# Optimization experiments

Hardware: AMD Instinct MI355X
Metric: run time of the kernel (lower is better)

The kernel has to match this reference:

```python
import jax, jax.numpy as jnp
import numpy as np

B, Lq, C, NH, NP, DFF = 8, 10000, 256, 8, 4, 1024
H_IMG, W_IMG = 100, 100
HD = C // NH


def _layer_norm(x, g, b, eps=1e-5):
    m = jnp.mean(x, -1, keepdims=True)
    v = jnp.mean((x - m) ** 2, -1, keepdims=True)
    return (x - m) / jnp.sqrt(v + eps) * g + b


def _bilinear_sample(value, loc, Hs, Ws):
    # value: [B, Lin, NH, HD]; loc: [B, Lq, NH, NP, 2] normalized to [0,1]
    vt = jnp.transpose(value, (0, 2, 1, 3))  # [B, NH, Lin, HD]
    # move to [B, NH, Lq, NP] layout once; grid_sample(align_corners=False) pixel coords
    x = jnp.transpose(loc[..., 0], (0, 2, 1, 3)) * Ws - 0.5
    y = jnp.transpose(loc[..., 1], (0, 2, 1, 3)) * Hs - 0.5
    x0 = jnp.floor(x); y0 = jnp.floor(y)
    lx = x - x0; ly = y - y0

    def corner(xi, yi, w):
        valid = (xi >= 0) & (xi < Ws) & (yi >= 0) & (yi < Hs)
        xc = jnp.clip(xi, 0, Ws - 1).astype(jnp.int32)
        yc = jnp.clip(yi, 0, Hs - 1).astype(jnp.int32)
        idx = (yc * Ws + xc).reshape(B, NH, Lq * NP, 1)
        v = jnp.take_along_axis(vt, idx, axis=2).reshape(B, NH, Lq, NP, HD)
        return v * (w * valid)[..., None]

    acc = corner(x0, y0, (1 - lx) * (1 - ly))
    acc = acc + corner(x0 + 1, y0, lx * (1 - ly))
    acc = acc + corner(x0, y0 + 1, (1 - lx) * ly)
    acc = acc + corner(x0 + 1, y0 + 1, lx * ly)
    return acc  # [B, NH, Lq, NP, HD]


def setup_inputs() -> dict:
    key = jax.random.key(0)
    ks = jax.random.split(key, 12)
    s = 0.02
    return {
        "query": jax.random.normal(ks[0], (B, Lq, C), jnp.float32),
        "src": jax.random.normal(ks[1], (B, H_IMG * W_IMG, C), jnp.float32),
        "reference_points": jax.random.uniform(ks[2], (B, Lq, 1, 2), jnp.float32),
        "spatial_shapes": jnp.array([[H_IMG, W_IMG]], dtype=jnp.int64),
        "level_start_index": jnp.array([0], dtype=jnp.int64),
        "W_off": jax.random.normal(ks[3], (C, NH * NP * 2), jnp.float32) * s,
        "b_off": jnp.zeros((NH * NP * 2,), jnp.float32),
        "W_aw": jax.random.normal(ks[4], (C, NH * NP), jnp.float32) * s,
        "b_aw": jnp.zeros((NH * NP,), jnp.float32),
        "W_val": jax.random.normal(ks[5], (C, C), jnp.float32) * s,
        "b_val": jnp.zeros((C,), jnp.float32),
        "W_out": jax.random.normal(ks[6], (C, C), jnp.float32) * s,
        "b_out": jnp.zeros((C,), jnp.float32),
        "g1": jnp.ones((C,), jnp.float32),
        "be1": jnp.zeros((C,), jnp.float32),
        "W1": jax.random.normal(ks[7], (C, DFF), jnp.float32) * s,
        "b1": jnp.zeros((DFF,), jnp.float32),
        "W2": jax.random.normal(ks[8], (DFF, C), jnp.float32) * s,
        "b2": jnp.zeros((C,), jnp.float32),
        "g2": jnp.ones((C,), jnp.float32),
        "be2": jnp.zeros((C,), jnp.float32),
    }


def reference(query, src, reference_points, spatial_shapes, level_start_index,
              W_off, b_off, W_aw, b_aw, W_val, b_val, W_out, b_out,
              g1, be1, W1, b1, W2, b2, g2, be2):
    Hs = spatial_shapes[0, 0]
    Ws = spatial_shapes[0, 1]
    # MSDeformAttn (n_levels = 1)
    value = (src @ W_val + b_val).reshape(B, -1, NH, HD)
    off = (query @ W_off + b_off).reshape(B, Lq, NH, NP, 2)
    aw = jax.nn.softmax((query @ W_aw + b_aw).reshape(B, Lq, NH, NP), axis=-1)
    normalizer = jnp.stack([Ws, Hs]).astype(query.dtype)  # (W, H)
    loc = reference_points[:, :, None] + off / normalizer  # [B,Lq,NH,NP,2]
    sampled = _bilinear_sample(value, loc, Hs, Ws)  # [B,NH,Lq,NP,HD]
    attn = jnp.einsum('bhqpd,bqhp->bqhd', sampled, aw).reshape(B, Lq, C)
    attn = attn @ W_out + b_out
    # residual + LN + FFN + LN
    q = _layer_norm(query + attn, g1, be1)
    ffn = jax.nn.relu(q @ W1 + b1) @ W2 + b2
    return _layer_norm(q + ffn, g2, be2)
```

## Files before the change

kernel.cpp:

```cpp
#include <hip/hip_runtime.h>
#include <hip/hip_bf16.h>

typedef __hip_bfloat16 bf16;
typedef unsigned short u16;
typedef short short8 __attribute__((ext_vector_type(8)));
typedef float f32x4 __attribute__((ext_vector_type(4)));

static constexpr int B_   = 8;
static constexpr int Lq_  = 10000;
static constexpr int C_   = 256;
static constexpr int NH_  = 8;
static constexpr int NP_  = 4;
static constexpr int DFF_ = 1024;
static constexpr int HIMG = 100;
static constexpr int WIMG = 100;
static constexpr int LIN  = 10000;

__device__ __forceinline__ u16 f2bf(float x) {
    union { bf16 b; u16 u; } cv; cv.b = __float2bfloat16(x); return cv.u;
}
__device__ __forceinline__ float bf2f(u16 u) {
    return __uint_as_float((unsigned)u << 16);
}
__device__ __forceinline__ void stf(float* p, float v) { *p = v; }
__device__ __forceinline__ void stf(u16* p, float v)   { *p = f2bf(v); }

__device__ __forceinline__ void gl_lds16(const void* g, void* l) {
    __builtin_amdgcn_global_load_lds(
        (const __attribute__((address_space(1))) void*)g,
        (__attribute__((address_space(3))) void*)l, 16, 0, 0);
}

template <bool RELU, bool AF32, typename TC>
__global__ __launch_bounds__(256) void gemm_mfma(
    const void* __restrict__ Av, const u16* __restrict__ Bt,
    const float* __restrict__ bias, TC* __restrict__ C,
    int M, int K, int Nreal, int ldc)
{
    __shared__ __align__(16) u16 As[2][128 * 32];
    __shared__ __align__(16) u16 Bs[2][128 * 32];

    const int tid  = threadIdx.x;
    const int lane = tid & 63;
    const int w    = tid >> 6;
    const int wr   = (w >> 1) * 64;
    const int wc   = (w & 1) * 64;
    const int m0   = blockIdx.y * 128;
    const int n0   = blockIdx.x * 128;

    const int srow = lane >> 2;
    const int scol = (lane & 3) << 3;
    const u16* bG = Bt + (size_t)(n0 + w * 32 + srow) * K + scol;
    const size_t rstep16 = (size_t)16 * K;

    const u16*   aG  = nullptr;
    const float* aGf = nullptr;
    int ar = 0, ac = 0;
    if constexpr (AF32) {
        ar  = lane >> 3;
        ac  = (lane & 7) << 2;
        aGf = (const float*)Av + (size_t)(m0 + w * 32 + ar) * K + ac;
    } else {
        aG = (const u16*)Av + (size_t)(m0 + w * 32 + srow) * K + scol;
    }

    const int aRoff = (wr + (lane & 15)) * 32 + (lane >> 4) * 8;
    const int bRoff = (wc + (lane & 15)) * 32 + (lane >> 4) * 8;

    f32x4 acc[4][4];
#pragma unroll
    for (int i = 0; i < 4; ++i)
#pragma unroll
        for (int j = 0; j < 4; ++j) acc[i][j] = f32x4{0.f, 0.f, 0.f, 0.f};

    float4 a4[4];

    const int nt = K >> 5;

    if constexpr (AF32) {
#pragma unroll
        for (int rep = 0; rep < 4; ++rep)
            a4[rep] = *(const float4*)(aGf + (size_t)(rep * 8) * K);
#pragma unroll
        for (int rep = 0; rep < 4; ++rep) {
            ushort4 v{f2bf(a4[rep].x), f2bf(a4[rep].y), f2bf(a4[rep].z), f2bf(a4[rep].w)};
            *(ushort4*)&As[0][(w * 32 + rep * 8 + ar) * 32 + ac] = v;
        }
    } else {
        gl_lds16(aG, &As[0][(w * 32) * 32]);
        gl_lds16(aG + rstep16, &As[0][(w * 32 + 16) * 32]);
    }
    gl_lds16(bG, &Bs[0][(w * 32) * 32]);
    gl_lds16(bG + rstep16, &Bs[0][(w * 32 + 16) * 32]);
    asm volatile("s_waitcnt vmcnt(0) lgkmcnt(0)" ::: "memory");
    __builtin_amdgcn_s_barrier();

    for (int t = 0; t < nt; ++t) {
        const int cur = t & 1;
        const int nxt = cur ^ 1;
        const int k0n = (t + 1) << 5;
        const bool has_next = (t + 1 < nt);

        if (has_next) {
            if constexpr (AF32) {
#pragma unroll
                for (int rep = 0; rep < 4; ++rep)
                    a4[rep] = *(const float4*)(aGf + k0n + (size_t)(rep * 8) * K);
            } else {
                gl_lds16(aG + k0n, &As[nxt][(w * 32) * 32]);
                gl_lds16(aG + k0n + rstep16, &As[nxt][(w * 32 + 16) * 32]);
            }
            gl_lds16(bG + k0n, &Bs[nxt][(w * 32) * 32]);
            gl_lds16(bG + k0n + rstep16, &Bs[nxt][(w * 32 + 16) * 32]);
        }

        short8 af[4], bfr[4];
#pragma unroll
        for (int m = 0; m < 4; ++m) af[m]  = *(const short8*)&As[cur][aRoff + m * 16 * 32];
#pragma unroll
        for (int n = 0; n < 4; ++n) bfr[n] = *(const short8*)&Bs[cur][bRoff + n * 16 * 32];
#pragma unroll
        for (int m = 0; m < 4; ++m)
#pragma unroll
            for (int n = 0; n < 4; ++n)
                acc[m][n] = __builtin_amdgcn_mfma_f32_16x16x32_bf16(
                    af[m], bfr[n], acc[m][n], 0, 0, 0);

        if constexpr (AF32) {
            if (has_next) {
#pragma unroll
                for (int rep = 0; rep < 4; ++rep) {
                    ushort4 v{f2bf(a4[rep].x), f2bf(a4[rep].y), f2bf(a4[rep].z), f2bf(a4[rep].w)};
                    *(ushort4*)&As[nxt][(w * 32 + rep * 8 + ar) * 32 + ac] = v;
                }
            }
        }

        asm volatile("s_waitcnt vmcnt(0) lgkmcnt(0)" ::: "memory");
        __builtin_amdgcn_s_barrier();
    }

#pragma unroll
    for (int n = 0; n < 4; ++n) {
        const int gc = n0 + wc + n * 16 + (lane & 15);
        if (gc >= Nreal) continue;
        const float bv = bias[gc];
        const int gr0 = m0 + wr + (lane >> 4) * 4;
#pragma unroll
        for (int m = 0; m < 4; ++m) {
#pragma unroll
            for (int r = 0; r < 4; ++r) {
                float v = acc[m][n][r] + bv;
                if (RELU) v = fmaxf(v, 0.f);
                stf(&C[(size_t)(gr0 + m * 16 + r) * ldc + gc], v);
            }
        }
    }
}

__global__ __launch_bounds__(256) void prep_all(
    const float* __restrict__ Wv, const float* __restrict__ Wo,
    const float* __restrict__ W1, const float* __restrict__ W2,
    const float* __restrict__ Woff, const float* __restrict__ Waw,
    const float* __restrict__ boff, const float* __restrict__ baw,
    u16* __restrict__ Wv_t, u16* __restrict__ Wo_t,
    u16* __restrict__ W1_t, u16* __restrict__ W2_t,
    u16* __restrict__ Woa_t, float* __restrict__ boa)
{
    const int idx = blockIdx.x * 256 + threadIdx.x;
    if (idx < 65536) {
        const int n = idx >> 8, k = idx & 255;
        Wv_t[idx] = f2bf(Wv[(size_t)k * 256 + n]);
    } else if (idx < 131072) {
        const int i = idx - 65536, n = i >> 8, k = i & 255;
        Wo_t[i] = f2bf(Wo[(size_t)k * 256 + n]);
    } else if (idx < 393216) {
        const int i = idx - 131072, n = i >> 8, k = i & 255;
        W1_t[i] = f2bf(W1[(size_t)k * 1024 + n]);
    } else if (idx < 655360) {
        const int i = idx - 393216, n = i >> 10, k = i & 1023;
        W2_t[i] = f2bf(W2[(size_t)k * 256 + n]);
    } else if (idx < 688128) {
        const int i = idx - 655360, n = i >> 8, k = i & 255;
        float v = 0.f;
        if (n < 64)      v = Woff[(size_t)k * 64 + n];
        else if (n < 96) v = Waw[(size_t)k * 32 + (n - 64)];
        Woa_t[i] = f2bf(v);
    } else if (idx < 688256) {
        const int i = idx - 688128;
        boa[i] = (i < 64) ? boff[i] : (i < 96 ? baw[i - 64] : 0.f);
    }
}

__global__ __launch_bounds__(256) void sample_attn(
    const u16* __restrict__ val, const float* __restrict__ oaw,
    const float* __restrict__ refp, u16* __restrict__ attn)
{
    const int t   = threadIdx.x;
    const int gid = blockIdx.x * 64 + (t >> 2);
    const int c0  = (t & 3) << 3;
    const int h   = gid & (NH_ - 1);
    const int bq  = gid >> 3;

    const float* row = oaw + (size_t)bq * 96;
    const float rx = refp[(size_t)bq * 2 + 0] * (float)WIMG;
    const float ry = refp[(size_t)bq * 2 + 1] * (float)HIMG;

    const float4 aw4 = *(const float4*)(row + 64 + h * 4);
    const float mx = fmaxf(fmaxf(aw4.x, aw4.y), fmaxf(aw4.z, aw4.w));
    const float e0 = __expf(aw4.x - mx), e1 = __expf(aw4.y - mx);
    const float e2 = __expf(aw4.z - mx), e3 = __expf(aw4.w - mx);
    const float inv = 1.f / (e0 + e1 + e2 + e3);
    const float w4[4] = {e0 * inv, e1 * inv, e2 * inv, e3 * inv};

    const int b = bq / Lq_;
    const u16* vb = val + (size_t)b * LIN * C_ + h * 32 + c0;

    float acc[8] = {};
#pragma unroll
    for (int p = 0; p < NP_; ++p) {
        const float2 off = *(const float2*)(row + (h * 4 + p) * 2);
        const float x = rx + off.x - 0.5f;
        const float y = ry + off.y - 0.5f;
        const float xf = floorf(x), yf = floorf(y);
        const float lx = x - xf, ly = y - yf;
        const int x0 = (int)xf, y0 = (int)yf;
        const float wp = w4[p];
        const float w00 = wp * (1.f - lx) * (1.f - ly);
        const float w10 = wp * lx * (1.f - ly);
        const float w01 = wp * (1.f - lx) * ly;
        const float w11 = wp * lx * ly;

#pragma unroll
        for (int c = 0; c < 4; ++c) {
            const int xi = x0 + (c & 1);
            const int yi = y0 + (c >> 1);
            const float wc = (c == 0) ? w00 : (c == 1) ? w10 : (c == 2) ? w01 : w11;
            const bool v = ((unsigned)xi < (unsigned)WIMG) & ((unsigned)yi < (unsigned)HIMG);
            const int idx = v ? (yi * WIMG + xi) : 0;
            const float w = v ? wc : 0.f;
            const short8 d = *(const short8*)(vb + (size_t)idx * C_);
#pragma unroll
            for (int j = 0; j < 8; ++j)
                acc[j] = fmaf(w, bf2f(((const u16*)&d)[j]), acc[j]);
        }
    }

    union { short8 s; u16 u[8]; } o;
#pragma unroll
    for (int j = 0; j < 8; ++j) o.u[j] = f2bf(acc[j]);
    *(short8*)(attn + (size_t)bq * C_ + h * 32 + c0) = o.s;
}

template <bool XF32, bool OUTF32>
__global__ __launch_bounds__(256) void ln_add(
    const void* __restrict__ xp, const u16* __restrict__ y,
    const float* __restrict__ g, const float* __restrict__ be,
    void* __restrict__ outp, int rows)
{
    const int row  = blockIdx.x * 4 + (threadIdx.x >> 6);
    const int lane = threadIdx.x & 63;
    if (row >= rows) return;

    float v[4];
    if constexpr (XF32) {
        const float4 xv = *(const float4*)((const float*)xp + (size_t)row * C_ + (lane << 2));
        v[0] = xv.x; v[1] = xv.y; v[2] = xv.z; v[3] = xv.w;
    } else {
        const ushort4 xv = *(const ushort4*)((const u16*)xp + (size_t)row * C_ + (lane << 2));
        v[0] = bf2f(xv.x); v[1] = bf2f(xv.y); v[2] = bf2f(xv.z); v[3] = bf2f(xv.w);
    }
    const ushort4 yv = *(const ushort4*)(y + (size_t)row * C_ + (lane << 2));
    v[0] += bf2f(yv.x); v[1] += bf2f(yv.y); v[2] += bf2f(yv.z); v[3] += bf2f(yv.w);

    float s  = v[0] + v[1] + v[2] + v[3];
    float s2 = v[0] * v[0] + v[1] * v[1] + v[2] * v[2] + v[3] * v[3];
#pragma unroll
    for (int o = 32; o >= 1; o >>= 1) {
        s  += __shfl_xor(s, o);
        s2 += __shfl_xor(s2, o);
    }
    const float mean = s * (1.f / 256.f);
    const float var  = fmaxf(s2 * (1.f / 256.f) - mean * mean, 0.f);
    const float rstd = rsqrtf(var + 1e-5f);

    const float4 gv = *(const float4*)(g  + (lane << 2));
    const float4 bv = *(const float4*)(be + (lane << 2));
    float o4[4];
    o4[0] = (v[0] - mean) * rstd * gv.x + bv.x;
    o4[1] = (v[1] - mean) * rstd * gv.y + bv.y;
    o4[2] = (v[2] - mean) * rstd * gv.z + bv.z;
    o4[3] = (v[3] - mean) * rstd * gv.w + bv.w;

    if constexpr (OUTF32) {
        float4 ov{o4[0], o4[1], o4[2], o4[3]};
        *(float4*)((float*)outp + (size_t)row * C_ + (lane << 2)) = ov;
    } else {
        ushort4 ov{f2bf(o4[0]), f2bf(o4[1]), f2bf(o4[2]), f2bf(o4[3])};
        *(ushort4*)((u16*)outp + (size_t)row * C_ + (lane << 2)) = ov;
    }
}

extern "C" void kernel_launch(void* const* d_in, const int* in_sizes, int n_in,
                              void* d_out, int out_size, void* d_ws, size_t ws_size,
                              hipStream_t stream)
{
    const float* query = (const float*)d_in[0];
    const float* src   = (const float*)d_in[1];
    const float* refp  = (const float*)d_in[2];
    const float* W_off = (const float*)d_in[5];
    const float* b_off = (const float*)d_in[6];
    const float* W_aw  = (const float*)d_in[7];
    const float* b_aw  = (const float*)d_in[8];
    const float* W_val = (const float*)d_in[9];
    const float* b_val = (const float*)d_in[10];
    const float* W_out = (const float*)d_in[11];
    const float* b_out = (const float*)d_in[12];
    const float* g1    = (const float*)d_in[13];
    const float* be1   = (const float*)d_in[14];
    const float* W1    = (const float*)d_in[15];
    const float* b1    = (const float*)d_in[16];
    const float* W2    = (const float*)d_in[17];
    const float* b2    = (const float*)d_in[18];
    const float* g2    = (const float*)d_in[19];
    const float* be2   = (const float*)d_in[20];
    float* out = (float*)d_out;

    char* ws = (char*)d_ws;
    const int R = B_ * Lq_;

    u16*  val   = (u16*)(ws + 0);
    u16*  ffno  = (u16*)(ws + 0);
    float* oaw  = (float*)(ws + 40960000);
    u16*  h     = (u16*)(ws + 40960000);
    u16*  attn  = (u16*)(ws + 71680000);
    u16*  attno = (u16*)(ws + 112640000);
    u16*  q1b   = (u16*)(ws + 204800000);
    u16*  Wv_t  = (u16*)(ws + 245760000);
    u16*  Wo_t  = (u16*)(ws + 245760000 + 131072);
    u16*  W1_t  = (u16*)(ws + 245760000 + 262144);
    u16*  W2_t  = (u16*)(ws + 245760000 + 786432);
    u16*  Woa_t = (u16*)(ws + 245760000 + 1310720);
    float* boa  = (float*)(ws + 245760000 + 1376256);

    const dim3 blk(256);

    prep_all<<<2689, blk, 0, stream>>>(W_val, W_out, W1, W2, W_off, W_aw,
                                       b_off, b_aw, Wv_t, Wo_t, W1_t, W2_t,
                                       Woa_t, boa);

    gemm_mfma<false, true, u16><<<dim3(2, 625), blk, 0, stream>>>(
        src, Wv_t, b_val, val, R, 256, 256, 256);
    gemm_mfma<false, true, float><<<dim3(1, 625), blk, 0, stream>>>(
        query, Woa_t, boa, oaw, R, 256, 96, 96);
    sample_attn<<<dim3(R * NH_ / 64), blk, 0, stream>>>(val, oaw, refp, attn);
    gemm_mfma<false, false, u16><<<dim3(2, 625), blk, 0, stream>>>(
        attn, Wo_t, b_out, attno, R, 256, 256, 256);
    ln_add<true, false><<<dim3(R / 4), blk, 0, stream>>>(
        query, attno, g1, be1, q1b, R);
    gemm_mfma<true, false, u16><<<dim3(8, 625), blk, 0, stream>>>(
        q1b, W1_t, b1, h, R, 256, 1024, 1024);
    gemm_mfma<false, false, u16><<<dim3(2, 625), blk, 0, stream>>>(
        h, W2_t, b2, ffno, R, 1024, 256, 256);
    ln_add<false, true><<<dim3(R / 4), blk, 0, stream>>>(
        q1b, ffno, g2, be2, out, R);
}
```

Measured before the change: 368.7 us.

## Fuse LayerNorm into GEMM epilogues and fuse FFN into one kernel

Replaces the generic GEMM with a 128x256 full-row tile kernel that can apply residual add and LayerNorm in its epilogue, so the separate ln_add passes and the attno intermediate go away. The two FFN GEMMs are fused into one kernel that keeps the hidden activation chunk in LDS, so the 80000x1024 bf16 intermediate is never written to or read back from global memory. LDS tiles use XOR swizzling, with weights pre-swizzled in prep, to avoid bank conflicts. The cost is heavy LDS use and more barriers per block, which may limit occupancy. The q1b layout is swizzled so that only the fused FFN kernel can read it.

```diff
diff --git a/kernel.cpp b/kernel.cpp
--- a/kernel.cpp
+++ b/kernel.cpp
@@ -11,7 +11,6 @@
 static constexpr int C_   = 256;
 static constexpr int NH_  = 8;
 static constexpr int NP_  = 4;
-static constexpr int DFF_ = 1024;
 static constexpr int HIMG = 100;
 static constexpr int WIMG = 100;
 static constexpr int LIN  = 10000;
@@ -22,23 +21,385 @@
 __device__ __forceinline__ float bf2f(u16 u) {
     return __uint_as_float((unsigned)u << 16);
 }
-__device__ __forceinline__ void stf(float* p, float v) { *p = v; }
-__device__ __forceinline__ void stf(u16* p, float v)   { *p = f2bf(v); }
 
 __device__ __forceinline__ void gl_lds16(const void* g, void* l) {
     __builtin_amdgcn_global_load_lds(
         (const __attribute__((address_space(1))) void*)g,
         (__attribute__((address_space(3))) void*)l, 16, 0, 0);
 }
-
-template <bool RELU, bool AF32, typename TC>
-__global__ __launch_bounds__(256) void gemm_mfma(
-    const void* __restrict__ Av, const u16* __restrict__ Bt,
-    const float* __restrict__ bias, TC* __restrict__ C,
+__device__ __forceinline__ void drain_barrier() {
+    asm volatile("s_waitcnt vmcnt(0) lgkmcnt(0)" ::: "memory");
+    __builtin_amdgcn_s_barrier();
+}
+
+
+template <bool AF32, bool LN>
+__global__ __launch_bounds__(512, 2) void gemm256(
+    const void* __restrict__ Av, const u16* __restrict__ Bg,
+    const float* __restrict__ bias, const float* __restrict__ resid,
+    const float* __restrict__ gw, const float* __restrict__ bw,
+    u16* __restrict__ Co, int K)
+{
+    __shared__ __align__(16) u16 At[2][128 * 64];
+    __shared__ __align__(16) u16 Bt[2][256 * 64];
+    __shared__ float red[2][128][4];
+
+    const int tid  = threadIdx.x;
+    const int lane = tid & 63;
+    const int w    = tid >> 6;
+    const int wm   = w >> 2, wn = w & 3;
+    const int m0   = blockIdx.x * 128;
+
+    f32x4 acc[4][4];
+#pragma unroll
+    for (int i = 0; i < 4; ++i)
+#pragma unroll
+        for (int j = 0; j < 4; ++j) acc[i][j] = f32x4{0.f, 0.f, 0.f, 0.f};
+
+    auto stageA = [&](int t) {
+        const int kt = t << 6;
+        if constexpr (AF32) {
+            const int row = tid >> 2;
+            const int k0  = (tid & 3) << 4;
+            const float* s = (const float*)Av + (size_t)(m0 + row) * K + kt + k0;
+            float4 v0 = *(const float4*)(s + 0);
+            float4 v1 = *(const float4*)(s + 4);
+            float4 v2 = *(const float4*)(s + 8);
+            float4 v3 = *(const float4*)(s + 12);
+            union { short8 s8; u16 u[8]; } ga, gb;
+            ga.u[0]=f2bf(v0.x); ga.u[1]=f2bf(v0.y); ga.u[2]=f2bf(v0.z); ga.u[3]=f2bf(v0.w);
+            ga.u[4]=f2bf(v1.x); ga.u[5]=f2bf(v1.y); ga.u[6]=f2bf(v1.z); ga.u[7]=f2bf(v1.w);
+            gb.u[0]=f2bf(v2.x); gb.u[1]=f2bf(v2.y); gb.u[2]=f2bf(v2.z); gb.u[3]=f2bf(v2.w);
+            gb.u[4]=f2bf(v3.x); gb.u[5]=f2bf(v3.y); gb.u[6]=f2bf(v3.z); gb.u[7]=f2bf(v3.w);
+            u16* d = &At[t & 1][row * 64];
+            *(short8*)&d[(k0)     ^ ((row & 7) << 3)] = ga.s8;
+            *(short8*)&d[(k0 + 8) ^ ((row & 7) << 3)] = gb.s8;
+        } else {
+#pragma unroll
+            for (int i = 0; i < 2; ++i) {
+                const int rb  = w * 16 + i * 8;
+                const int row = rb + (lane >> 3);
+                const int gs  = (lane & 7) ^ (row & 7);
+                gl_lds16((const u16*)Av + (size_t)(m0 + row) * K + kt + gs * 8,
+                         &At[t & 1][rb * 64]);
+            }
+        }
+    };
+    auto stageB = [&](int t) {
+        const int kt = t << 6;
+#pragma unroll
+        for (int i = 0; i < 4; ++i) {
+            const int rb  = w * 32 + i * 8;
+            const int row = rb + (lane >> 3);
+            gl_lds16(Bg + (size_t)row * K + kt + (lane & 7) * 8,
+                     &Bt[t & 1][rb * 64]);
+        }
+    };
+    auto compute = [&](int t) {
+        const u16* a = At[t & 1];
+        const u16* b = Bt[t & 1];
+#pragma unroll
+        for (int ks = 0; ks < 2; ++ks) {
+            const int ko = ks * 32 + ((lane >> 4) << 3);
+            short8 bfr[4];
+#pragma unroll
+            for (int n = 0; n < 4; ++n) {
+                const int nr = wn * 64 + n * 16 + (lane & 15);
+                bfr[n] = *(const short8*)&b[nr * 64 + (ko ^ ((nr & 7) << 3))];
+            }
+#pragma unroll
+            for (int m = 0; m < 4; ++m) {
+                const int ar = wm * 64 + m * 16 + (lane & 15);
+                const short8 af = *(const short8*)&a[ar * 64 + (ko ^ ((ar & 7) << 3))];
+#pragma unroll
+                for (int n = 0; n < 4; ++n)
+                    acc[m][n] = __builtin_amdgcn_mfma_f32_16x16x32_bf16(
+                        af, bfr[n], acc[m][n], 0, 0, 0);
+            }
+        }
+    };
+
+    stageA(0); stageB(0);
+    drain_barrier();
+    const int nt = K >> 6;
+    for (int t = 0; t < nt; ++t) {
+        if (t + 1 < nt) { stageA(t + 1); stageB(t + 1); }
+        compute(t);
+        drain_barrier();
+    }
+
+    float bcol[4], gcol[4], becol[4];
+#pragma unroll
+    for (int n = 0; n < 4; ++n) {
+        const int col = wn * 64 + n * 16 + (lane & 15);
+        bcol[n] = bias[col];
+        if (LN) { gcol[n] = gw[col]; becol[n] = bw[col]; }
+    }
+
+    if constexpr (!LN) {
+#pragma unroll
+        for (int m = 0; m < 4; ++m)
+#pragma unroll
+            for (int r = 0; r < 4; ++r) {
+                const int lr = wm * 64 + m * 16 + (lane >> 4) * 4 + r;
+#pragma unroll
+                for (int n = 0; n < 4; ++n) {
+                    const int col = wn * 64 + n * 16 + (lane & 15);
+                    Co[(size_t)(m0 + lr) * 256 + col] = f2bf(acc[m][n][r] + bcol[n]);
+                }
+            }
+    } else {
+        float s[4][4], s2[4][4];
+#pragma unroll
+        for (int m = 0; m < 4; ++m)
+#pragma unroll
+            for (int r = 0; r < 4; ++r) {
+                const int lr = wm * 64 + m * 16 + (lane >> 4) * 4 + r;
+                float ps = 0.f, ps2 = 0.f;
+#pragma unroll
+                for (int n = 0; n < 4; ++n) {
+                    const int col = wn * 64 + n * 16 + (lane & 15);
+                    float v = acc[m][n][r] + bcol[n]
+                            + resid[(size_t)(m0 + lr) * 256 + col];
+                    acc[m][n][r] = v;
+                    ps += v; ps2 += v * v;
+                }
+#pragma unroll
+                for (int o = 1; o < 16; o <<= 1) {
+                    ps  += __shfl_xor(ps,  o);
+                    ps2 += __shfl_xor(ps2, o);
+                }
+                s[m][r] = ps; s2[m][r] = ps2;
+            }
+        if ((lane & 15) == 0) {
+#pragma unroll
+            for (int m = 0; m < 4; ++m)
+#pragma unroll
+                for (int r = 0; r < 4; ++r) {
+                    const int lr = wm * 64 + m * 16 + (lane >> 4) * 4 + r;
+                    red[0][lr][wn] = s[m][r];
+                    red[1][lr][wn] = s2[m][r];
+                }
+        }
+        __syncthreads();
+        if (tid < 128) {
+            const float ss  = red[0][tid][0] + red[0][tid][1] + red[0][tid][2] + red[0][tid][3];
+            const float ss2 = red[1][tid][0] + red[1][tid][1] + red[1][tid][2] + red[1][tid][3];
+            const float mean = ss * (1.f / 256.f);
+            const float var  = fmaxf(ss2 * (1.f / 256.f) - mean * mean, 0.f);
+            red[0][tid][0] = mean;
+            red[1][tid][0] = rsqrtf(var + 1e-5f);
+        }
+        __syncthreads();
+#pragma unroll
+        for (int m = 0; m < 4; ++m)
+#pragma unroll
+            for (int r = 0; r < 4; ++r) {
+                const int lr = wm * 64 + m * 16 + (lane >> 4) * 4 + r;
+                const float mean = red[0][lr][0];
+                const float rstd = red[1][lr][0];
+#pragma unroll
+                for (int n = 0; n < 4; ++n) {
+                    const int col = wn * 64 + n * 16 + (lane & 15);
+                    const float o = (acc[m][n][r] - mean) * rstd * gcol[n] + becol[n];
+                    Co[(size_t)(m0 + lr) * 256 + (col ^ ((lr & 7) << 3))] = f2bf(o);
+                }
+            }
+    }
+}
+
+__global__ __launch_bounds__(512, 2) void ffn_fused(
+    const u16* __restrict__ q1b, const u16* __restrict__ W1s,
+    const u16* __restrict__ W2s, const float* __restrict__ b1,
+    const float* __restrict__ b2, const float* __restrict__ g2,
+    const float* __restrict__ be2, float* __restrict__ out)
+{
+    __shared__ __align__(16) u16 As[128 * 256];
+    __shared__ __align__(16) u16 Hs[128 * 128];
+    __shared__ __align__(16) u16 B1t[2][128 * 32];
+    __shared__ __align__(16) u16 B2t[2][256 * 32];
+    __shared__ float red[2][128][4];
+
+    const int tid  = threadIdx.x;
+    const int lane = tid & 63;
+    const int w    = tid >> 6;
+    const int wm   = w >> 2, wn = w & 3;
+    const int m0   = blockIdx.x * 128;
+
+    f32x4 acc2[4][4];
+#pragma unroll
+    for (int i = 0; i < 4; ++i)
+#pragma unroll
+        for (int j = 0; j < 4; ++j) acc2[i][j] = f32x4{0.f, 0.f, 0.f, 0.f};
+
+    auto stageB1 = [&](int c, int t) {
+        const int rb  = w * 16;
+        const int row = rb + (lane >> 2);
+        gl_lds16(W1s + (size_t)(c * 128 + row) * 256 + t * 32 + (lane & 3) * 8,
+                 &B1t[t & 1][rb * 32]);
+    };
+    auto stageB2 = [&](int c, int t) {
+#pragma unroll
+        for (int i = 0; i < 2; ++i) {
+            const int rb  = i * 128 + w * 16;
+            const int row = rb + (lane >> 2);
+            gl_lds16(W2s + (size_t)row * 1024 + c * 128 + t * 32 + (lane & 3) * 8,
+                     &B2t[t & 1][rb * 32]);
+        }
+    };
+
+#pragma unroll
+    for (int i = 0; i < 8; ++i) {
+        const int rb = w * 16 + i * 2;
+        gl_lds16(q1b + (size_t)(m0 + rb + (lane >> 5)) * 256 + (lane & 31) * 8,
+                 &As[rb * 256]);
+    }
+    stageB1(0, 0);
+    drain_barrier();
+
+    for (int c = 0; c < 8; ++c) {
+        f32x4 acc1[4][2];
+#pragma unroll
+        for (int i = 0; i < 4; ++i)
+#pragma unroll
+            for (int j = 0; j < 2; ++j) acc1[i][j] = f32x4{0.f, 0.f, 0.f, 0.f};
+
+        for (int t = 0; t < 8; ++t) {
+            if (t < 7) stageB1(c, t + 1);
+            else       stageB2(c, 0);
+            const u16* b = B1t[t & 1];
+            const int ko = (lane >> 4) << 3;
+            short8 bfr[2];
+#pragma unroll
+            for (int n = 0; n < 2; ++n) {
+                const int nr = wn * 32 + n * 16 + (lane & 15);
+                bfr[n] = *(const short8*)&b[nr * 32 + (ko ^ ((nr & 3) << 3))];
+            }
+#pragma unroll
+            for (int m = 0; m < 4; ++m) {
+                const int ar = wm * 64 + m * 16 + (lane & 15);
+                const short8 af = *(const short8*)
+                    &As[ar * 256 + ((t * 32 + ko) ^ ((ar & 7) << 3))];
+#pragma unroll
+                for (int n = 0; n < 2; ++n)
+                    acc1[m][n] = __builtin_amdgcn_mfma_f32_16x16x32_bf16(
+                        af, bfr[n], acc1[m][n], 0, 0, 0);
+            }
+            drain_barrier();
+        }
+
+#pragma unroll
+        for (int n = 0; n < 2; ++n) {
+            const int col = wn * 32 + n * 16 + (lane & 15);
+            const float bb = b1[c * 128 + col];
+#pragma unroll
+            for (int m = 0; m < 4; ++m)
+#pragma unroll
+                for (int r = 0; r < 4; ++r) {
+                    const int row = wm * 64 + m * 16 + (lane >> 4) * 4 + r;
+                    const float hv = fmaxf(acc1[m][n][r] + bb, 0.f);
+                    Hs[row * 128 + (col ^ ((row & 7) << 3))] = f2bf(hv);
+                }
+        }
+        asm volatile("s_waitcnt lgkmcnt(0)" ::: "memory");
+        __builtin_amdgcn_s_barrier();
+
+        for (int t = 0; t < 4; ++t) {
+            if (t < 3)      stageB2(c, t + 1);
+            else if (c < 7) stageB1(c + 1, 0);
+            const u16* b = B2t[t & 1];
+            const int ko = (lane >> 4) << 3;
+            short8 bfr[4];
+#pragma unroll
+            for (int n = 0; n < 4; ++n) {
+                const int nr = wn * 64 + n * 16 + (lane & 15);
+                bfr[n] = *(const short8*)&b[nr * 32 + (ko ^ ((nr & 3) << 3))];
+            }
+#pragma unroll
+            for (int m = 0; m < 4; ++m) {
+                const int hr = wm * 64 + m * 16 + (lane & 15);
+                const short8 af = *(const short8*)
+                    &Hs[hr * 128 + ((t * 32 + ko) ^ ((hr & 7) << 3))];
+#pragma unroll
+                for (int n = 0; n < 4; ++n)
+                    acc2[m][n] = __builtin_amdgcn_mfma_f32_16x16x32_bf16(
+                        af, bfr[n], acc2[m][n], 0, 0, 0);
+            }
+            drain_barrier();
+        }
+    }
+
+    float bcol[4], gcol[4], becol[4];
+#pragma unroll
+    for (int n = 0; n < 4; ++n) {
+        const int col = wn * 64 + n * 16 + (lane & 15);
+        bcol[n] = b2[col]; gcol[n] = g2[col]; becol[n] = be2[col];
+    }
+    float s[4][4], s2[4][4];
+#pragma unroll
+    for (int m = 0; m < 4; ++m)
+#pragma unroll
+        for (int r = 0; r < 4; ++r) {
+            const int lr = wm * 64 + m * 16 + (lane >> 4) * 4 + r;
+            float ps = 0.f, ps2 = 0.f;
+#pragma unroll
+            for (int n = 0; n < 4; ++n) {
+                const int col = wn * 64 + n * 16 + (lane & 15);
+                const float q = bf2f(As[lr * 256 + (col ^ ((lr & 7) << 3))]);
+                const float v = acc2[m][n][r] + bcol[n] + q;
+                acc2[m][n][r] = v;
+                ps += v; ps2 += v * v;
+            }
+#pragma unroll
+            for (int o = 1; o < 16; o <<= 1) {
+                ps  += __shfl_xor(ps,  o);
+                ps2 += __shfl_xor(ps2, o);
+            }
+            s[m][r] = ps; s2[m][r] = ps2;
+        }
+    if ((lane & 15) == 0) {
+#pragma unroll
+        for (int m = 0; m < 4; ++m)
+#pragma unroll
+            for (int r = 0; r < 4; ++r) {
+                const int lr = wm * 64 + m * 16 + (lane >> 4) * 4 + r;
+                red[0][lr][wn] = s[m][r];
+                red[1][lr][wn] = s2[m][r];
+            }
+    }
+    __syncthreads();
+    if (tid < 128) {
+        const float ss  = red[0][tid][0] + red[0][tid][1] + red[0][tid][2] + red[0][tid][3];
+        const float ss2 = red[1][tid][0] + red[1][tid][1] + red[1][tid][2] + red[1][tid][3];
+        const float mean = ss * (1.f / 256.f);
+        const float var  = fmaxf(ss2 * (1.f / 256.f) - mean * mean, 0.f);
+        red[0][tid][0] = mean;
+        red[1][tid][0] = rsqrtf(var + 1e-5f);
+    }
+    __syncthreads();
+#pragma unroll
+    for (int m = 0; m < 4; ++m)
+#pragma unroll
+        for (int r = 0; r < 4; ++r) {
+            const int lr = wm * 64 + m * 16 + (lane >> 4) * 4 + r;
+            const float mean = red[0][lr][0];
+            const float rstd = red[1][lr][0];
+#pragma unroll
+            for (int n = 0; n < 4; ++n) {
+                const int col = wn * 64 + n * 16 + (lane & 15);
+                out[(size_t)(m0 + lr) * 256 + col] =
+                    (acc2[m][n][r] - mean) * rstd * gcol[n] + becol[n];
+            }
+        }
+}
+
+__global__ __launch_bounds__(256) void gemm_oaw(
+    const float* __restrict__ Av, const u16* __restrict__ Bt,
+    const float* __restrict__ bias, float* __restrict__ C,
     int M, int K, int Nreal, int ldc)
 {
-    __shared__ __align__(16) u16 As[2][128 * 32];
-    __shared__ __align__(16) u16 Bs[2][128 * 32];
+    __shared__ __align__(16) u16 Asl[2][128 * 32];
+    __shared__ __align__(16) u16 Bsl[2][128 * 32];
 
     const int tid  = threadIdx.x;
     const int lane = tid & 63;
@@ -53,16 +414,9 @@
     const u16* bG = Bt + (size_t)(n0 + w * 32 + srow) * K + scol;
     const size_t rstep16 = (size_t)16 * K;
 
-    const u16*   aG  = nullptr;
-    const float* aGf = nullptr;
-    int ar = 0, ac = 0;
-    if constexpr (AF32) {
-        ar  = lane >> 3;
-        ac  = (lane & 7) << 2;
-        aGf = (const float*)Av + (size_t)(m0 + w * 32 + ar) * K + ac;
-    } else {
-        aG = (const u16*)Av + (size_t)(m0 + w * 32 + srow) * K + scol;
-    }
+    const int ar  = lane >> 3;
+    const int ac  = (lane & 7) << 2;
+    const float* aGf = Av + (size_t)(m0 + w * 32 + ar) * K + ac;
 
     const int aRoff = (wr + (lane & 15)) * 32 + (lane >> 4) * 8;
     const int bRoff = (wc + (lane & 15)) * 32 + (lane >> 4) * 8;
@@ -74,70 +428,50 @@
         for (int j = 0; j < 4; ++j) acc[i][j] = f32x4{0.f, 0.f, 0.f, 0.f};
 
     float4 a4[4];
-
     const int nt = K >> 5;
 
-    if constexpr (AF32) {
-#pragma unroll
-        for (int rep = 0; rep < 4; ++rep)
-            a4[rep] = *(const float4*)(aGf + (size_t)(rep * 8) * K);
-#pragma unroll
-        for (int rep = 0; rep < 4; ++rep) {
-            ushort4 v{f2bf(a4[rep].x), f2bf(a4[rep].y), f2bf(a4[rep].z), f2bf(a4[rep].w)};
-            *(ushort4*)&As[0][(w * 32 + rep * 8 + ar) * 32 + ac] = v;
-        }
-    } else {
-        gl_lds16(aG, &As[0][(w * 32) * 32]);
-        gl_lds16(aG + rstep16, &As[0][(w * 32 + 16) * 32]);
-    }
-    gl_lds16(bG, &Bs[0][(w * 32) * 32]);
-    gl_lds16(bG + rstep16, &Bs[0][(w * 32 + 16) * 32]);
-    asm volatile("s_waitcnt vmcnt(0) lgkmcnt(0)" ::: "memory");
-    __builtin_amdgcn_s_barrier();
+#pragma unroll
+    for (int rep = 0; rep < 4; ++rep)
+        a4[rep] = *(const float4*)(aGf + (size_t)(rep * 8) * K);
+#pragma unroll
+    for (int rep = 0; rep < 4; ++rep) {
+        ushort4 v{f2bf(a4[rep].x), f2bf(a4[rep].y), f2bf(a4[rep].z), f2bf(a4[rep].w)};
+        *(ushort4*)&Asl[0][(w * 32 + rep * 8 + ar) * 32 + ac] = v;
+    }
+    gl_lds16(bG, &Bsl[0][(w * 32) * 32]);
+    gl_lds16(bG + rstep16, &Bsl[0][(w * 32 + 16) * 32]);
+    drain_barrier();
 
     for (int t = 0; t < nt; ++t) {
-        const int cur = t & 1;
-        const int nxt = cur ^ 1;
+        const int cur = t & 1, nxt = cur ^ 1;
         const int k0n = (t + 1) << 5;
         const bool has_next = (t + 1 < nt);
-
         if (has_next) {
-            if constexpr (AF32) {
-#pragma unroll
-                for (int rep = 0; rep < 4; ++rep)
-                    a4[rep] = *(const float4*)(aGf + k0n + (size_t)(rep * 8) * K);
-            } else {
-                gl_lds16(aG + k0n, &As[nxt][(w * 32) * 32]);
-                gl_lds16(aG + k0n + rstep16, &As[nxt][(w * 32 + 16) * 32]);
-            }
-            gl_lds16(bG + k0n, &Bs[nxt][(w * 32) * 32]);
-            gl_lds16(bG + k0n + rstep16, &Bs[nxt][(w * 32 + 16) * 32]);
-        }
-
+#pragma unroll
+            for (int rep = 0; rep < 4; ++rep)
+                a4[rep] = *(const float4*)(aGf + k0n + (size_t)(rep * 8) * K);
+            gl_lds16(bG + k0n, &Bsl[nxt][(w * 32) * 32]);
+            gl_lds16(bG + k0n + rstep16, &Bsl[nxt][(w * 32 + 16) * 32]);
+        }
         short8 af[4], bfr[4];
 #pragma unroll
-        for (int m = 0; m < 4; ++m) af[m]  = *(const short8*)&As[cur][aRoff + m * 16 * 32];
-#pragma unroll
-        for (int n = 0; n < 4; ++n) bfr[n] = *(const short8*)&Bs[cur][bRoff + n * 16 * 32];
+        for (int m = 0; m < 4; ++m) af[m]  = *(const short8*)&Asl[cur][aRoff + m * 16 * 32];
+#pragma unroll
+        for (int n = 0; n < 4; ++n) bfr[n] = *(const short8*)&Bsl[cur][bRoff + n * 16 * 32];
 #pragma unroll
         for (int m = 0; m < 4; ++m)
 #pragma unroll
             for (int n = 0; n < 4; ++n)
                 acc[m][n] = __builtin_amdgcn_mfma_f32_16x16x32_bf16(
                     af[m], bfr[n], acc[m][n], 0, 0, 0);
-
-        if constexpr (AF32) {
-            if (has_next) {
-#pragma unroll
-                for (int rep = 0; rep < 4; ++rep) {
-                    ushort4 v{f2bf(a4[rep].x), f2bf(a4[rep].y), f2bf(a4[rep].z), f2bf(a4[rep].w)};
-                    *(ushort4*)&As[nxt][(w * 32 + rep * 8 + ar) * 32 + ac] = v;
-                }
-            }
-        }
-
-        asm volatile("s_waitcnt vmcnt(0) lgkmcnt(0)" ::: "memory");
-        __builtin_amdgcn_s_barrier();
+        if (has_next) {
+#pragma unroll
+            for (int rep = 0; rep < 4; ++rep) {
+                ushort4 v{f2bf(a4[rep].x), f2bf(a4[rep].y), f2bf(a4[rep].z), f2bf(a4[rep].w)};
+                *(ushort4*)&Asl[nxt][(w * 32 + rep * 8 + ar) * 32 + ac] = v;
+            }
+        }
+        drain_barrier();
     }
 
 #pragma unroll
@@ -147,14 +481,10 @@
         const float bv = bias[gc];
         const int gr0 = m0 + wr + (lane >> 4) * 4;
 #pragma unroll
-        for (int m = 0; m < 4; ++m) {
-#pragma unroll
-            for (int r = 0; r < 4; ++r) {
-                float v = acc[m][n][r] + bv;
-                if (RELU) v = fmaxf(v, 0.f);
-                stf(&C[(size_t)(gr0 + m * 16 + r) * ldc + gc], v);
-            }
-        }
+        for (int m = 0; m < 4; ++m)
+#pragma unroll
+            for (int r = 0; r < 4; ++r)
+                C[(size_t)(gr0 + m * 16 + r) * ldc + gc] = acc[m][n][r] + bv;
     }
 }
 
@@ -163,29 +493,29 @@
     const float* __restrict__ W1, const float* __restrict__ W2,
     const float* __restrict__ Woff, const float* __restrict__ Waw,
     const float* __restrict__ boff, const float* __restrict__ baw,
-    u16* __restrict__ Wv_t, u16* __restrict__ Wo_t,
-    u16* __restrict__ W1_t, u16* __restrict__ W2_t,
-    u16* __restrict__ Woa_t, float* __restrict__ boa)
+    u16* __restrict__ Wvs, u16* __restrict__ Wos,
+    u16* __restrict__ W1s, u16* __restrict__ W2s,
+    u16* __restrict__ Woa, float* __restrict__ boa)
 {
     const int idx = blockIdx.x * 256 + threadIdx.x;
     if (idx < 65536) {
-        const int n = idx >> 8, k = idx & 255;
-        Wv_t[idx] = f2bf(Wv[(size_t)k * 256 + n]);
+        const int n = idx >> 8, kd = idx & 255;
+        Wvs[idx] = f2bf(Wv[(size_t)(kd ^ ((n & 7) << 3)) * 256 + n]);
     } else if (idx < 131072) {
-        const int i = idx - 65536, n = i >> 8, k = i & 255;
-        Wo_t[i] = f2bf(Wo[(size_t)k * 256 + n]);
+        const int i = idx - 65536, n = i >> 8, kd = i & 255;
+        Wos[i] = f2bf(Wo[(size_t)(kd ^ ((n & 7) << 3)) * 256 + n]);
     } else if (idx < 393216) {
-        const int i = idx - 131072, n = i >> 8, k = i & 255;
-        W1_t[i] = f2bf(W1[(size_t)k * 1024 + n]);
+        const int i = idx - 131072, n = i >> 8, kd = i & 255;
+        W1s[i] = f2bf(W1[(size_t)(kd ^ ((n & 3) << 3)) * 1024 + n]);
     } else if (idx < 655360) {
-        const int i = idx - 393216, n = i >> 10, k = i & 1023;
-        W2_t[i] = f2bf(W2[(size_t)k * 256 + n]);
+        const int i = idx - 393216, n = i >> 10, kd = i & 1023;
+        W2s[i] = f2bf(W2[(size_t)(kd ^ ((n & 3) << 3)) * 256 + n]);
     } else if (idx < 688128) {
         const int i = idx - 655360, n = i >> 8, k = i & 255;
         float v = 0.f;
         if (n < 64)      v = Woff[(size_t)k * 64 + n];
         else if (n < 96) v = Waw[(size_t)k * 32 + (n - 64)];
-        Woa_t[i] = f2bf(v);
+        Woa[i] = f2bf(v);
     } else if (idx < 688256) {
         const int i = idx - 688128;
         boa[i] = (i < 64) ? boff[i] : (i < 96 ? baw[i - 64] : 0.f);
@@ -250,55 +580,6 @@
 #pragma unroll
     for (int j = 0; j < 8; ++j) o.u[j] = f2bf(acc[j]);
     *(short8*)(attn + (size_t)bq * C_ + h * 32 + c0) = o.s;
-}
-
-template <bool XF32, bool OUTF32>
-__global__ __launch_bounds__(256) void ln_add(
-    const void* __restrict__ xp, const u16* __restrict__ y,
-    const float* __restrict__ g, const float* __restrict__ be,
-    void* __restrict__ outp, int rows)
-{
-    const int row  = blockIdx.x * 4 + (threadIdx.x >> 6);
-    const int lane = threadIdx.x & 63;
-    if (row >= rows) return;
-
-    float v[4];
-    if constexpr (XF32) {
-        const float4 xv = *(const float4*)((const float*)xp + (size_t)row * C_ + (lane << 2));
-        v[0] = xv.x; v[1] = xv.y; v[2] = xv.z; v[3] = xv.w;
-    } else {
-        const ushort4 xv = *(const ushort4*)((const u16*)xp + (size_t)row * C_ + (lane << 2));
-        v[0] = bf2f(xv.x); v[1] = bf2f(xv.y); v[2] = bf2f(xv.z); v[3] = bf2f(xv.w);
-    }
-    const ushort4 yv = *(const ushort4*)(y + (size_t)row * C_ + (lane << 2));
-    v[0] += bf2f(yv.x); v[1] += bf2f(yv.y); v[2] += bf2f(yv.z); v[3] += bf2f(yv.w);
-
-    float s  = v[0] + v[1] + v[2] + v[3];
-    float s2 = v[0] * v[0] + v[1] * v[1] + v[2] * v[2] + v[3] * v[3];
-#pragma unroll
-    for (int o = 32; o >= 1; o >>= 1) {
-        s  += __shfl_xor(s, o);
-        s2 += __shfl_xor(s2, o);
-    }
-    const float mean = s * (1.f / 256.f);
-    const float var  = fmaxf(s2 * (1.f / 256.f) - mean * mean, 0.f);
-    const float rstd = rsqrtf(var + 1e-5f);
-
-    const float4 gv = *(const float4*)(g  + (lane << 2));
-    const float4 bv = *(const float4*)(be + (lane << 2));
-    float o4[4];
-    o4[0] = (v[0] - mean) * rstd * gv.x + bv.x;
-    o4[1] = (v[1] - mean) * rstd * gv.y + bv.y;
-    o4[2] = (v[2] - mean) * rstd * gv.z + bv.z;
-    o4[3] = (v[3] - mean) * rstd * gv.w + bv.w;
-
-    if constexpr (OUTF32) {
-        float4 ov{o4[0], o4[1], o4[2], o4[3]};
-        *(float4*)((float*)outp + (size_t)row * C_ + (lane << 2)) = ov;
-    } else {
-        ushort4 ov{f2bf(o4[0]), f2bf(o4[1]), f2bf(o4[2]), f2bf(o4[3])};
-        *(ushort4*)((u16*)outp + (size_t)row * C_ + (lane << 2)) = ov;
-    }
 }
 
 extern "C" void kernel_launch(void* const* d_in, const int* in_sizes, int n_in,
@@ -329,39 +610,31 @@
     char* ws = (char*)d_ws;
     const int R = B_ * Lq_;
 
-    u16*  val   = (u16*)(ws + 0);
-    u16*  ffno  = (u16*)(ws + 0);
-    float* oaw  = (float*)(ws + 40960000);
-    u16*  h     = (u16*)(ws + 40960000);
-    u16*  attn  = (u16*)(ws + 71680000);
-    u16*  attno = (u16*)(ws + 112640000);
-    u16*  q1b   = (u16*)(ws + 204800000);
-    u16*  Wv_t  = (u16*)(ws + 245760000);
-    u16*  Wo_t  = (u16*)(ws + 245760000 + 131072);
-    u16*  W1_t  = (u16*)(ws + 245760000 + 262144);
-    u16*  W2_t  = (u16*)(ws + 245760000 + 786432);
-    u16*  Woa_t = (u16*)(ws + 245760000 + 1310720);
-    float* boa  = (float*)(ws + 245760000 + 1376256);
-
-    const dim3 blk(256);
-
-    prep_all<<<2689, blk, 0, stream>>>(W_val, W_out, W1, W2, W_off, W_aw,
-                                       b_off, b_aw, Wv_t, Wo_t, W1_t, W2_t,
-                                       Woa_t, boa);
-
-    gemm_mfma<false, true, u16><<<dim3(2, 625), blk, 0, stream>>>(
-        src, Wv_t, b_val, val, R, 256, 256, 256);
-    gemm_mfma<false, true, float><<<dim3(1, 625), blk, 0, stream>>>(
-        query, Woa_t, boa, oaw, R, 256, 96, 96);
-    sample_attn<<<dim3(R * NH_ / 64), blk, 0, stream>>>(val, oaw, refp, attn);
-    gemm_mfma<false, false, u16><<<dim3(2, 625), blk, 0, stream>>>(
-        attn, Wo_t, b_out, attno, R, 256, 256, 256);
-    ln_add<true, false><<<dim3(R / 4), blk, 0, stream>>>(
-        query, attno, g1, be1, q1b, R);
-    gemm_mfma<true, false, u16><<<dim3(8, 625), blk, 0, stream>>>(
-        q1b, W1_t, b1, h, R, 256, 1024, 1024);
-    gemm_mfma<false, false, u16><<<dim3(2, 625), blk, 0, stream>>>(
-        h, W2_t, b2, ffno, R, 1024, 256, 256);
-    ln_add<false, true><<<dim3(R / 4), blk, 0, stream>>>(
-        q1b, ffno, g2, be2, out, R);
-}
+    u16*  val  = (u16*)(ws + 0);
+    float* oaw = (float*)(ws + 40960000);
+    u16*  attn = (u16*)(ws + 71680000);
+    u16*  q1b  = (u16*)(ws + 112640000);
+    u16*  Wvs  = (u16*)(ws + 153600000);
+    u16*  Wos  = (u16*)(ws + 153600000 + 131072);
+    u16*  W1s  = (u16*)(ws + 153600000 + 262144);
+    u16*  W2s  = (u16*)(ws + 153600000 + 786432);
+    u16*  Woa  = (u16*)(ws + 153600000 + 1310720);
+    float* boa = (float*)(ws + 153600000 + 1376256);
+
+    prep_all<<<2689, 256, 0, stream>>>(W_val, W_out, W1, W2, W_off, W_aw,
+                                       b_off, b_aw, Wvs, Wos, W1s, W2s,
+                                       Woa, boa);
+
+    gemm256<true, false><<<625, 512, 0, stream>>>(
+        src, Wvs, b_val, nullptr, nullptr, nullptr, val, 256);
+
+    gemm_oaw<<<dim3(1, 625), 256, 0, stream>>>(
+        query, Woa, boa, oaw, R, 256, 96, 96);
+
+    sample_attn<<<10000, 256, 0, stream>>>(val, oaw, refp, attn);
+
+    gemm256<false, true><<<625, 512, 0, stream>>>(
+        attn, Wos, b_out, query, g1, be1, q1b, 256);
+
+    ffn_fused<<<625, 512, 0, stream>>>(q1b, W1s, W2s, b1, b2, g2, be2, out);
+}
```

Result: faster. 327.4 us (-11.2%).
